# Kernel tuning notes

Measured on AMD Instinct MI355X. Metric: run time of the kernel, lower is better.

## Reference

```python
import jax, jax.numpy as jnp
import numpy as np

NEG_SLOPE = 0.2  # PyG GATConv default leaky_relu slope


def _gat_layer(x, src, dst, n_nodes, W, a_src, a_dst, b, heads, out_ch):
    # x: [N, Fin] -> h: [N, H, C]
    h = (x @ W).reshape(n_nodes, heads, out_ch)
    alpha_s = jnp.einsum('nhc,hc->nh', h, a_src)  # [N, H]
    alpha_d = jnp.einsum('nhc,hc->nh', h, a_dst)  # [N, H]
    e = jax.nn.leaky_relu(alpha_s[src] + alpha_d[dst], NEG_SLOPE)  # [E, H]
    # segment softmax over edges grouped by destination node
    m = jax.ops.segment_max(e, dst, num_segments=n_nodes)          # [N, H]
    e = jnp.exp(e - m[dst])
    denom = jax.ops.segment_sum(e, dst, num_segments=n_nodes)      # [N, H]
    alpha = e / denom[dst]                                          # self-loops guarantee denom > 0
    msg = alpha[:, :, None] * h[src]                                # [E, H, C]
    out = jax.ops.segment_sum(msg, dst, num_segments=n_nodes)      # [N, H, C]
    return out.reshape(n_nodes, heads * out_ch) + b


def reference(x, edge_index, batch, W1, a_src1, a_dst1, b1, W2, a_src2, a_dst2, b2, fc_w, fc_b):
    n_nodes = x.shape[0]
    heads = a_src1.shape[0]
    # PyG GATConv adds self-loops by default
    loops = jnp.arange(n_nodes, dtype=edge_index.dtype)
    src = jnp.concatenate([edge_index[0], loops])
    dst = jnp.concatenate([edge_index[1], loops])

    h = _gat_layer(x, src, dst, n_nodes, W1, a_src1, a_dst1, b1, heads, 64)
    h = jax.nn.relu(h)  # dropout is identity in eval mode
    h = _gat_layer(h, src, dst, n_nodes, W2, a_src2, a_dst2, b2, heads, 16)
    h = jax.nn.relu(h)

    n_graphs = 64
    sums = jax.ops.segment_sum(h, batch, num_segments=n_graphs)                    # [G, 64]
    counts = jax.ops.segment_sum(jnp.ones((n_nodes,), h.dtype), batch, num_segments=n_graphs)
    pooled = sums / jnp.maximum(counts, 1.0)[:, None]                              # global_mean_pool
    return pooled @ fc_w + fc_b


def setup_inputs() -> dict:
    key = jax.random.key(0)
    ks = jax.random.split(key, 12)
    N, E, F_in, G = 50000, 800000, 128, 64
    H = 4
    x = jax.random.normal(ks[0], (N, F_in), jnp.float32)
    edge_index = jax.random.randint(ks[1], (2, E), 0, N, jnp.int32)
    batch = jnp.sort(jax.random.randint(ks[2], (N,), 0, G, jnp.int32))
    s1 = 1.0 / np.sqrt(F_in)
    s2 = 1.0 / np.sqrt(H * 64)
    s3 = 1.0 / np.sqrt(H * 16)
    return {
        'x': x,
        'edge_index': edge_index,
        'batch': batch,
        'W1': jax.random.normal(ks[3], (F_in, H * 64), jnp.float32) * s1,
        'a_src1': jax.random.normal(ks[4], (H, 64), jnp.float32) * s1,
        'a_dst1': jax.random.normal(ks[5], (H, 64), jnp.float32) * s1,
        'b1': jnp.zeros((H * 64,), jnp.float32),
        'W2': jax.random.normal(ks[6], (H * 64, H * 16), jnp.float32) * s2,
        'a_src2': jax.random.normal(ks[7], (H, 16), jnp.float32) * s2,
        'a_dst2': jax.random.normal(ks[8], (H, 16), jnp.float32) * s2,
        'b2': jnp.zeros((H * 16,), jnp.float32),
        'fc_w': jax.random.normal(ks[9], (H * 16, 32), jnp.float32) * s3,
        'fc_b': jnp.zeros((32,), jnp.float32),
    }
```

## Files before the change

### kernel.cpp

```cpp
#include <hip/hip_runtime.h>
#include <hip/hip_bf16.h>
#include <hip/hip_fp16.h>
#include <math.h>

#define HEADS 4
#define CAP 64

typedef _Float16 half8_t __attribute__((ext_vector_type(8)));
typedef float float4_t __attribute__((ext_vector_type(4)));


__global__ void zero_cnt_k(int* cnt, int N) {
    int i = blockIdx.x * blockDim.x + threadIdx.x;
    if (i < N) cnt[i] = 0;
}


__global__ void cvt_w1t_k(const float* __restrict__ W1, _Float16* __restrict__ BT) {
    int k = blockIdx.x;
    int n = threadIdx.x;
    BT[n * 128 + k] = (_Float16)W1[k * 256 + n];
}

__global__ void cvt_w2t_k(const float* __restrict__ W2, _Float16* __restrict__ BT) {
    int n = blockIdx.x;
    int k = threadIdx.x;
    BT[n * 256 + k] = (_Float16)W2[k * 64 + n];
}


__global__ __launch_bounds__(256) void fused_scatter_gemm1_k(
    const int* __restrict__ src, const int* __restrict__ dst,
    int* __restrict__ cnt, unsigned short* __restrict__ slots, int E, int N, int SB,
    const float* __restrict__ A,
    const _Float16* __restrict__ BT,
    __half* __restrict__ hout,
    const float* __restrict__ avs,
    const float* __restrict__ avd,
    float* __restrict__ os,
    float* __restrict__ od, int M) {
    __shared__ _Float16 lds[4 * 16 * 72];

    if ((int)blockIdx.x < SB) {
        int total = E + N;
        int T = SB * 256;
        int t0 = blockIdx.x * 256 + threadIdx.x;
        int d[4], s[4];
        #pragma unroll
        for (int k = 0; k < 4; k++) {
            int i = t0 + k * T;
            if (i < total) {
                if (i < E) { d[k] = dst[i]; s[k] = src[i]; }
                else       { d[k] = i - E;  s[k] = i - E; }
            } else d[k] = -1;
        }
        int p[4];
        #pragma unroll
        for (int k = 0; k < 4; k++) {
            if (d[k] >= 0) p[k] = atomicAdd(&cnt[d[k]], 1);
        }
        #pragma unroll
        for (int k = 0; k < 4; k++) {
            if (d[k] >= 0 && p[k] < CAP)
                slots[(size_t)d[k] * CAP + p[k]] = (unsigned short)s[k];
        }
        return;
    }

    int bx = blockIdx.x - SB;
    int wave = threadIdx.x >> 6;
    int lane = threadIdx.x & 63;
    int q = lane >> 4;
    int c16 = lane & 15;
    int row0 = bx * 64 + wave * 16;

    half8_t a[4];
    int ar = row0 + c16;
    bool avalid = (ar < M);
    const float* ap = A + (size_t)ar * 128;
    #pragma unroll
    for (int ks = 0; ks < 4; ks++) {
        if (avalid) {
            float4 f0 = *(const float4*)(ap + ks * 32 + q * 8);
            float4 f1 = *(const float4*)(ap + ks * 32 + q * 8 + 4);
            half8_t h;
            h[0] = (_Float16)f0.x; h[1] = (_Float16)f0.y;
            h[2] = (_Float16)f0.z; h[3] = (_Float16)f0.w;
            h[4] = (_Float16)f1.x; h[5] = (_Float16)f1.y;
            h[6] = (_Float16)f1.z; h[7] = (_Float16)f1.w;
            a[ks] = h;
        } else {
            a[ks] = (half8_t)(_Float16)0.0f;
        }
    }

    float4_t acc[16];
    #pragma unroll
    for (int ct = 0; ct < 16; ct++) acc[ct] = (float4_t)0.f;

    #pragma unroll
    for (int ks = 0; ks < 4; ks++) {
        #pragma unroll
        for (int ct = 0; ct < 16; ct++) {
            half8_t b = *(const half8_t*)(BT + (size_t)(ct * 16 + c16) * 128 + ks * 32 + q * 8);
            acc[ct] = __builtin_amdgcn_mfma_f32_16x16x32_f16(a[ks], b, acc[ct], 0, 0, 0);
        }
    }

    float psh[4][4] = {}, pdh[4][4] = {};
    #pragma unroll
    for (int ct = 0; ct < 16; ct++) {
        int h = ct >> 2;
        int cih = (ct & 3) * 16 + c16;
        float as_v = avs[h * 64 + cih];
        float ad_v = avd[h * 64 + cih];
        #pragma unroll
        for (int r = 0; r < 4; r++) {
            psh[h][r] = fmaf(acc[ct][r], as_v, psh[h][r]);
            pdh[h][r] = fmaf(acc[ct][r], ad_v, pdh[h][r]);
        }
    }
    #pragma unroll
    for (int h = 0; h < 4; h++) {
        #pragma unroll
        for (int r = 0; r < 4; r++) {
            #pragma unroll
            for (int o = 8; o >= 1; o >>= 1) {
                psh[h][r] += __shfl_down(psh[h][r], o, 16);
                pdh[h][r] += __shfl_down(pdh[h][r], o, 16);
            }
        }
    }
    if (c16 == 0) {
        #pragma unroll
        for (int r = 0; r < 4; r++) {
            int gr = row0 + q * 4 + r;
            if (gr < M) {
                #pragma unroll
                for (int h = 0; h < 4; h++) {
                    os[(size_t)gr * HEADS + h] = psh[h][r];
                    od[(size_t)gr * HEADS + h] = pdh[h][r];
                }
            }
        }
    }

    _Float16* wl = lds + wave * (16 * 72);
    #pragma unroll
    for (int chunk = 0; chunk < 4; chunk++) {
        #pragma unroll
        for (int c4 = 0; c4 < 4; c4++) {
            int ct = chunk * 4 + c4;
            #pragma unroll
            for (int r = 0; r < 4; r++) {
                wl[(q * 4 + r) * 72 + c4 * 16 + c16] = (_Float16)acc[ct][r];
            }
        }
        __syncthreads();
        #pragma unroll
        for (int pass = 0; pass < 2; pass++) {
            int idx8 = pass * 64 + lane;
            int row = idx8 >> 3;
            int col8 = idx8 & 7;
            int gr = row0 + row;
            if (gr < M) {
                *(half8_t*)(hout + (size_t)gr * 256 + chunk * 64 + col8 * 8) =
                    *(const half8_t*)(wl + row * 72 + col8 * 8);
            }
        }
        __syncthreads();
    }
}


__global__ __launch_bounds__(256) void mfma_gemm2_k(
    const _Float16* __restrict__ Ah,
    const _Float16* __restrict__ BT,
    __half* __restrict__ hout,
    const float* __restrict__ avs,
    const float* __restrict__ avd,
    float* __restrict__ os,
    float* __restrict__ od, int M) {
    __shared__ _Float16 lds[4 * 16 * 64];
    int wave = threadIdx.x >> 6;
    int lane = threadIdx.x & 63;
    int q = lane >> 4;
    int c16 = lane & 15;
    int row0 = blockIdx.x * 64 + wave * 16;

    half8_t a[8];
    int ar = row0 + c16;
    bool avalid = (ar < M);
    const _Float16* ap = Ah + (size_t)ar * 256;
    #pragma unroll
    for (int ks = 0; ks < 8; ks++) {
        if (avalid) a[ks] = *(const half8_t*)(ap + ks * 32 + q * 8);
        else        a[ks] = (half8_t)(_Float16)0.0f;
    }

    float4_t acc[4];
    #pragma unroll
    for (int ct = 0; ct < 4; ct++) acc[ct] = (float4_t)0.f;

    #pragma unroll
    for (int ks = 0; ks < 8; ks++) {
        #pragma unroll
        for (int ct = 0; ct < 4; ct++) {
            half8_t b = *(const half8_t*)(BT + (size_t)(ct * 16 + c16) * 256 + ks * 32 + q * 8);
            acc[ct] = __builtin_amdgcn_mfma_f32_16x16x32_f16(a[ks], b, acc[ct], 0, 0, 0);
        }
    }

    float ps[4][4], pd[4][4];
    #pragma unroll
    for (int ct = 0; ct < 4; ct++) {
        float as_v = avs[ct * 16 + c16];
        float ad_v = avd[ct * 16 + c16];
        #pragma unroll
        for (int r = 0; r < 4; r++) {
            ps[ct][r] = acc[ct][r] * as_v;
            pd[ct][r] = acc[ct][r] * ad_v;
            #pragma unroll
            for (int o = 8; o >= 1; o >>= 1) {
                ps[ct][r] += __shfl_down(ps[ct][r], o, 16);
                pd[ct][r] += __shfl_down(pd[ct][r], o, 16);
            }
        }
    }
    if (c16 == 0) {
        #pragma unroll
        for (int r = 0; r < 4; r++) {
            int gr = row0 + q * 4 + r;
            if (gr < M) {
                #pragma unroll
                for (int ct = 0; ct < 4; ct++) {
                    os[(size_t)gr * HEADS + ct] = ps[ct][r];
                    od[(size_t)gr * HEADS + ct] = pd[ct][r];
                }
            }
        }
    }

    _Float16* wl = lds + wave * (16 * 64);
    #pragma unroll
    for (int ct = 0; ct < 4; ct++) {
        #pragma unroll
        for (int r = 0; r < 4; r++) {
            wl[(q * 4 + r) * 64 + ct * 16 + c16] = (_Float16)acc[ct][r];
        }
    }
    __syncthreads();
    #pragma unroll
    for (int pass = 0; pass < 2; pass++) {
        int idx8 = pass * 64 + lane;
        int row = idx8 >> 3;
        int col8 = idx8 & 7;
        int gr = row0 + row;
        if (gr < M) {
            *(half8_t*)(hout + (size_t)gr * 64 + col8 * 8) =
                *(const half8_t*)(wl + row * 64 + col8 * 8);
        }
    }
}


__global__ __launch_bounds__(256) void gat_agg64_f16_k(
    const __half* __restrict__ hsrc,
    const float* __restrict__ as,
    const float* __restrict__ ad,
    const int* __restrict__ cnt,
    const unsigned short* __restrict__ slots,
    const float* __restrict__ bias,
    __half* __restrict__ outh,
    int N) {
    int node = blockIdx.x * 4 + (threadIdx.x >> 6);
    if (node >= N) return;
    int l = threadIdx.x & 63;
    int h = l >> 4;
    int je = l & 15;
    int hb = h << 4;
    int deg = min(cnt[node], CAP);
    const unsigned short* sp = slots + (size_t)node * CAP;
    float adh = ad[(size_t)node * HEADS + h];
    float4 bv = *(const float4*)(bias + l * 4);
    float m = -INFINITY, den = 0.f;
    float4 acc = make_float4(0.f, 0.f, 0.f, 0.f);
    for (int base = 0; base < deg; base += 16) {
        int cl = min(16, deg - base);
        int s = 0;
        float e = -INFINITY;
        if (je < cl) {
            s = sp[base + je];
            float a = as[(size_t)s * HEADS + h] + adh;
            e = (a > 0.f) ? a : 0.2f * a;
        }
        float cmax = e;
        #pragma unroll
        for (int o = 8; o >= 1; o >>= 1) cmax = fmaxf(cmax, __shfl_xor(cmax, o));
        float m_new = fmaxf(m, cmax);
        float p = (je < cl) ? __expf(e - m_new) : 0.f;
        float sum = p;
        #pragma unroll
        for (int o = 8; o >= 1; o >>= 1) sum += __shfl_xor(sum, o);
        float sc = __expf(m - m_new);
        den = den * sc + sum;
        m = m_new;
        acc.x *= sc; acc.y *= sc; acc.z *= sc; acc.w *= sc;
        int j = 0;
        for (; j + 4 <= cl; j += 4) {
            float p0 = __shfl(p, hb + j),     p1 = __shfl(p, hb + j + 1);
            float p2 = __shfl(p, hb + j + 2), p3 = __shfl(p, hb + j + 3);
            int s0 = __shfl(s, hb + j),     s1 = __shfl(s, hb + j + 1);
            int s2 = __shfl(s, hb + j + 2), s3 = __shfl(s, hb + j + 3);
            uint2 r0 = *(const uint2*)(hsrc + (size_t)s0 * 256 + l * 4);
            uint2 r1 = *(const uint2*)(hsrc + (size_t)s1 * 256 + l * 4);
            uint2 r2 = *(const uint2*)(hsrc + (size_t)s2 * 256 + l * 4);
            uint2 r3 = *(const uint2*)(hsrc + (size_t)s3 * 256 + l * 4);
            float2 a0 = __half22float2(*(__half2*)&r0.x), b0 = __half22float2(*(__half2*)&r0.y);
            float2 a1 = __half22float2(*(__half2*)&r1.x), b1 = __half22float2(*(__half2*)&r1.y);
            float2 a2 = __half22float2(*(__half2*)&r2.x), b2 = __half22float2(*(__half2*)&r2.y);
            float2 a3 = __half22float2(*(__half2*)&r3.x), b3 = __half22float2(*(__half2*)&r3.y);
            acc.x = fmaf(p0, a0.x, acc.x); acc.y = fmaf(p0, a0.y, acc.y);
            acc.z = fmaf(p0, b0.x, acc.z); acc.w = fmaf(p0, b0.y, acc.w);
            acc.x = fmaf(p1, a1.x, acc.x); acc.y = fmaf(p1, a1.y, acc.y);
            acc.z = fmaf(p1, b1.x, acc.z); acc.w = fmaf(p1, b1.y, acc.w);
            acc.x = fmaf(p2, a2.x, acc.x); acc.y = fmaf(p2, a2.y, acc.y);
            acc.z = fmaf(p2, b2.x, acc.z); acc.w = fmaf(p2, b2.y, acc.w);
            acc.x = fmaf(p3, a3.x, acc.x); acc.y = fmaf(p3, a3.y, acc.y);
            acc.z = fmaf(p3, b3.x, acc.z); acc.w = fmaf(p3, b3.y, acc.w);
        }
        for (; j < cl; j++) {
            float pj = __shfl(p, hb + j);
            int sj = __shfl(s, hb + j);
            uint2 r0 = *(const uint2*)(hsrc + (size_t)sj * 256 + l * 4);
            float2 a0 = __half22float2(*(__half2*)&r0.x), b0 = __half22float2(*(__half2*)&r0.y);
            acc.x = fmaf(pj, a0.x, acc.x); acc.y = fmaf(pj, a0.y, acc.y);
            acc.z = fmaf(pj, b0.x, acc.z); acc.w = fmaf(pj, b0.y, acc.w);
        }
    }
    float inv = 1.f / den;
    float rx = fmaxf(fmaf(acc.x, inv, bv.x), 0.f);
    float ry = fmaxf(fmaf(acc.y, inv, bv.y), 0.f);
    float rz = fmaxf(fmaf(acc.z, inv, bv.z), 0.f);
    float rw = fmaxf(fmaf(acc.w, inv, bv.w), 0.f);
    __half2* op = (__half2*)(outh + (size_t)node * 256 + l * 4);
    op[0] = __floats2half2_rn(rx, ry);
    op[1] = __floats2half2_rn(rz, rw);
}


__global__ __launch_bounds__(256) void gat_agg16_f16_k(
    const __half* __restrict__ hsrc,
    const float* __restrict__ as,
    const float* __restrict__ ad,
    const int* __restrict__ cnt,
    const unsigned short* __restrict__ slots,
    const float* __restrict__ bias,
    float* __restrict__ out, int N) {
    int node = blockIdx.x * 4 + (threadIdx.x >> 6);
    if (node >= N) return;
    int l = threadIdx.x & 63;
    int ha = l >> 4;
    int je = l & 15;
    int q = l & 15;
    int hh = q >> 2;
    int eg = l >> 4;
    int deg = min(cnt[node], CAP);
    const unsigned short* sp = slots + (size_t)node * CAP;
    float adh = ad[(size_t)node * HEADS + ha];
    float m = -INFINITY, den = 0.f;
    float4 acc = make_float4(0.f, 0.f, 0.f, 0.f);
    for (int base = 0; base < deg; base += 16) {
        int cl = min(16, deg - base);
        int s = 0;
        float e = -INFINITY;
        if (je < cl) {
            s = sp[base + je];
            float a = as[(size_t)s * HEADS + ha] + adh;
            e = (a > 0.f) ? a : 0.2f * a;
        }
        float cmax = e;
        #pragma unroll
        for (int o = 8; o >= 1; o >>= 1) cmax = fmaxf(cmax, __shfl_xor(cmax, o));
        float m_new = fmaxf(m, cmax);
        float p = (je < cl) ? __expf(e - m_new) : 0.f;
        float sum = p;
        #pragma unroll
        for (int o = 8; o >= 1; o >>= 1) sum += __shfl_xor(sum, o);
        float sc = __expf(m - m_new);
        den = den * sc + sum;
        m = m_new;
        float sch = __shfl(sc, hh << 4);
        acc.x *= sch; acc.y *= sch; acc.z *= sch; acc.w *= sch;
        for (int j0 = 0; j0 < cl; j0 += 4) {
            int j = j0 + eg;
            int jc = min(j, cl - 1);
            float pj = __shfl(p, (hh << 4) + jc);
            int sj = __shfl(s, (hh << 4) + jc);
            if (j < cl) {
                uint2 raw = *(const uint2*)(hsrc + (size_t)sj * 64 + q * 4);
                float2 f0 = __half22float2(*(__half2*)&raw.x);
                float2 f1 = __half22float2(*(__half2*)&raw.y);
                acc.x = fmaf(pj, f0.x, acc.x); acc.y = fmaf(pj, f0.y, acc.y);
                acc.z = fmaf(pj, f1.x, acc.z); acc.w = fmaf(pj, f1.y, acc.w);
            }
        }
    }
    acc.x += __shfl_xor(acc.x, 16); acc.y += __shfl_xor(acc.y, 16);
    acc.z += __shfl_xor(acc.z, 16); acc.w += __shfl_xor(acc.w, 16);
    acc.x += __shfl_xor(acc.x, 32); acc.y += __shfl_xor(acc.y, 32);
    acc.z += __shfl_xor(acc.z, 32); acc.w += __shfl_xor(acc.w, 32);
    float denh = __shfl(den, hh << 4);
    if (eg == 0) {
        float inv = 1.f / denh;
        float4 bv = *(const float4*)(bias + q * 4);
        float4 r;
        r.x = fmaxf(fmaf(acc.x, inv, bv.x), 0.f);
        r.y = fmaxf(fmaf(acc.y, inv, bv.y), 0.f);
        r.z = fmaxf(fmaf(acc.z, inv, bv.z), 0.f);
        r.w = fmaxf(fmaf(acc.w, inv, bv.w), 0.f);
        *(float4*)(out + (size_t)node * 64 + q * 4) = r;
    }
}


__global__ void graph_bounds_k(const int* __restrict__ batch, int N, int* __restrict__ bstart) {
    int g = threadIdx.x;
    if (g <= 64) {
        int lo = 0, hi = N;
        while (lo < hi) {
            int mid = (lo + hi) >> 1;
            if (batch[mid] < g) lo = mid + 1; else hi = mid;
        }
        bstart[g] = lo;
    }
}

__global__ void pool_zero_k(float* __restrict__ sums) {
    sums[blockIdx.x * blockDim.x + threadIdx.x] = 0.f;
}

__global__ __launch_bounds__(256) void pool_sum_k(const float* __restrict__ g2,
                                                  const int* __restrict__ batch,
                                                  float* __restrict__ sums, int N) {
    int c = threadIdx.x & 63;
    int r = threadIdx.x >> 6;
    int base = blockIdx.x * 256;
    int lim = min(base + 256, N);
    float acc = 0.f;
    int cur = -1;
    for (int n = base + r; n < lim; n += 4) {
        int g = batch[n];
        if (g != cur) {
            if (cur >= 0) atomicAdd(&sums[cur * 64 + c], acc);
            acc = 0.f;
            cur = g;
        }
        acc += g2[(size_t)n * 64 + c];
    }
    if (cur >= 0) atomicAdd(&sums[cur * 64 + c], acc);
}

__global__ void fc_k(const float* __restrict__ sums, const int* __restrict__ bstart,
                     const float* __restrict__ w, const float* __restrict__ b,
                     float* __restrict__ out) {
    int g = blockIdx.x, o = threadIdx.x;
    float cnt_ = (float)max(bstart[g + 1] - bstart[g], 1);
    float inv = 1.f / cnt_;
    float acc = b[o];
    for (int k = 0; k < 64; k++) acc = fmaf(sums[g * 64 + k] * inv, w[k * 32 + o], acc);
    out[g * 32 + o] = acc;
}


static inline size_t align_up(size_t x, size_t a) { return (x + a - 1) & ~(a - 1); }

extern "C" void kernel_launch(void* const* d_in, const int* in_sizes, int n_in,
                              void* d_out, int out_size, void* d_ws, size_t ws_size,
                              hipStream_t stream) {
    const float* x      = (const float*)d_in[0];
    const int*   ei     = (const int*)d_in[1];
    const int*   batch  = (const int*)d_in[2];
    const float* W1     = (const float*)d_in[3];
    const float* a_src1 = (const float*)d_in[4];
    const float* a_dst1 = (const float*)d_in[5];
    const float* b1     = (const float*)d_in[6];
    const float* W2     = (const float*)d_in[7];
    const float* a_src2 = (const float*)d_in[8];
    const float* a_dst2 = (const float*)d_in[9];
    const float* b2     = (const float*)d_in[10];
    const float* fc_w   = (const float*)d_in[11];
    const float* fc_b   = (const float*)d_in[12];
    float* out = (float*)d_out;

    const int N = in_sizes[2];
    const int E = in_sizes[1] / 2;
    const int F_in = in_sizes[0] / N;
    const int D1 = HEADS * 64;
    const int D2 = HEADS * 16;

    const int* src = ei;
    const int* dst = ei + E;

    char* w = (char*)d_ws;
    size_t off = 0;
    auto alloc = [&](size_t bytes) {
        size_t p = off;
        off = align_up(off + bytes, 256);
        return (void*)(w + p);
    };
    int* cnt    = (int*)alloc((size_t)N * 4);
    unsigned short* slots = (unsigned short*)alloc((size_t)N * CAP * 2);
    int* bstart = (int*)alloc(65 * 4);
    float* pooled = (float*)alloc(64 * 64 * 4);
    float* as1  = (float*)alloc((size_t)N * HEADS * 4);
    float* ad1  = (float*)alloc((size_t)N * HEADS * 4);
    float* as2  = (float*)alloc((size_t)N * HEADS * 4);
    float* ad2  = (float*)alloc((size_t)N * HEADS * 4);
    __half* h1h = (__half*)alloc((size_t)N * D1 * 2);
    __half* g1h = (__half*)alloc((size_t)N * D1 * 2);
    __half* h2h = (__half*)alloc((size_t)N * D2 * 2);
    float* g2   = (float*)alloc((size_t)N * D2 * 4);
    _Float16* w1t = (_Float16*)alloc((size_t)F_in * D1 * 2);
    _Float16* w2t = (_Float16*)alloc((size_t)D1 * D2 * 2);

    zero_cnt_k<<<(N + 255) / 256, 256, 0, stream>>>(cnt, N);
    cvt_w1t_k<<<F_in, D1, 0, stream>>>(W1, w1t);
    cvt_w2t_k<<<D2, D1, 0, stream>>>(W2, w2t);

    const int SB = (E + N + 1023) / 1024;
    const int GB = (N + 63) / 64;
    fused_scatter_gemm1_k<<<SB + GB, 256, 0, stream>>>(
        src, dst, cnt, slots, E, N, SB,
        x, w1t, h1h, a_src1, a_dst1, as1, ad1, N);

    gat_agg64_f16_k<<<(N + 3) / 4, 256, 0, stream>>>(h1h, as1, ad1, cnt, slots, b1, g1h, N);

    mfma_gemm2_k<<<(N + 63) / 64, 256, 0, stream>>>((const _Float16*)g1h, w2t, h2h,
                                                    a_src2, a_dst2, as2, ad2, N);
    gat_agg16_f16_k<<<(N + 3) / 4, 256, 0, stream>>>(h2h, as2, ad2, cnt, slots, b2, g2, N);

    graph_bounds_k<<<1, 128, 0, stream>>>(batch, N, bstart);
    pool_zero_k<<<16, 256, 0, stream>>>(pooled);
    pool_sum_k<<<(N + 255) / 256, 256, 0, stream>>>(g2, batch, pooled, N);
    fc_k<<<64, 32, 0, stream>>>(pooled, bstart, fc_w, fc_b, out);
}
```

Baseline: 336.4 us.

## Partition edge scatter by destination range and pre-insert self-loops in init

```diff
diff --git a/kernel.cpp b/kernel.cpp
--- a/kernel.cpp
+++ b/kernel.cpp
@@ -10,9 +10,12 @@
 typedef float float4_t __attribute__((ext_vector_type(4)));
 
 
-__global__ void zero_cnt_k(int* cnt, int N) {
+__global__ void init_cnt_k(int* cnt, unsigned short* slots, int N) {
     int i = blockIdx.x * blockDim.x + threadIdx.x;
-    if (i < N) cnt[i] = 0;
+    if (i < N) {
+        cnt[i] = 1;
+        slots[(size_t)i * CAP] = (unsigned short)i;
+    }
 }
 
 
@@ -42,27 +45,19 @@
     __shared__ _Float16 lds[4 * 16 * 72];
 
     if ((int)blockIdx.x < SB) {
-        int total = E + N;
-        int T = SB * 256;
-        int t0 = blockIdx.x * 256 + threadIdx.x;
-        int d[4], s[4];
-        #pragma unroll
-        for (int k = 0; k < 4; k++) {
-            int i = t0 + k * T;
-            if (i < total) {
-                if (i < E) { d[k] = dst[i]; s[k] = src[i]; }
-                else       { d[k] = i - E;  s[k] = i - E; }
-            } else d[k] = -1;
-        }
-        int p[4];
-        #pragma unroll
-        for (int k = 0; k < 4; k++) {
-            if (d[k] >= 0) p[k] = atomicAdd(&cnt[d[k]], 1);
-        }
-        #pragma unroll
-        for (int k = 0; k < 4; k++) {
-            if (d[k] >= 0 && p[k] < CAP)
-                slots[(size_t)d[k] * CAP + p[k]] = (unsigned short)s[k];
+        int p = blockIdx.x & 7;
+        int bp = blockIdx.x >> 3;
+        int SBP = SB >> 3;
+        int T = SBP * 256;
+        int pstart = (int)(((long long)p * N) >> 3);
+        int pend   = (int)(((long long)(p + 1) * N) >> 3);
+        for (int i = bp * 256 + (int)threadIdx.x; i < E; i += T) {
+            int d = dst[i];
+            int s = src[i];
+            if (d >= pstart && d < pend) {
+                int pos = atomicAdd(&cnt[d], 1);
+                if (pos < CAP) slots[(size_t)d * CAP + pos] = (unsigned short)s;
+            }
         }
         return;
     }
@@ -524,11 +519,11 @@
     _Float16* w1t = (_Float16*)alloc((size_t)F_in * D1 * 2);
     _Float16* w2t = (_Float16*)alloc((size_t)D1 * D2 * 2);
 
-    zero_cnt_k<<<(N + 255) / 256, 256, 0, stream>>>(cnt, N);
+    init_cnt_k<<<(N + 255) / 256, 256, 0, stream>>>(cnt, slots, N);
     cvt_w1t_k<<<F_in, D1, 0, stream>>>(W1, w1t);
     cvt_w2t_k<<<D2, D1, 0, stream>>>(W2, w2t);
 
-    const int SB = (E + N + 1023) / 1024;
+    const int SB = 832;
     const int GB = (N + 63) / 64;
     fused_scatter_gemm1_k<<<SB + GB, 256, 0, stream>>>(
         src, dst, cnt, slots, E, N, SB,
```

Result: no change. 333.3 us (-0.9%).

## Split layer-1 aggregation per head across XCDs and pre-insert self-loops

Applied to the files above, without the earlier changes.

```diff
diff --git a/kernel.cpp b/kernel.cpp
--- a/kernel.cpp
+++ b/kernel.cpp
@@ -10,9 +10,12 @@
 typedef float float4_t __attribute__((ext_vector_type(4)));
 
 
-__global__ void zero_cnt_k(int* cnt, int N) {
+__global__ void init_cnt_k(int* cnt, unsigned short* slots, int N) {
     int i = blockIdx.x * blockDim.x + threadIdx.x;
-    if (i < N) cnt[i] = 0;
+    if (i < N) {
+        cnt[i] = 1;
+        slots[(size_t)i * CAP] = (unsigned short)i;
+    }
 }
 
 
@@ -31,7 +34,7 @@
 
 __global__ __launch_bounds__(256) void fused_scatter_gemm1_k(
     const int* __restrict__ src, const int* __restrict__ dst,
-    int* __restrict__ cnt, unsigned short* __restrict__ slots, int E, int N, int SB,
+    int* __restrict__ cnt, unsigned short* __restrict__ slots, int E, int SB,
     const float* __restrict__ A,
     const _Float16* __restrict__ BT,
     __half* __restrict__ hout,
@@ -42,25 +45,22 @@
     __shared__ _Float16 lds[4 * 16 * 72];
 
     if ((int)blockIdx.x < SB) {
-        int total = E + N;
         int T = SB * 256;
         int t0 = blockIdx.x * 256 + threadIdx.x;
-        int d[4], s[4];
-        #pragma unroll
-        for (int k = 0; k < 4; k++) {
+        int d[8], s[8];
+        #pragma unroll
+        for (int k = 0; k < 8; k++) {
             int i = t0 + k * T;
-            if (i < total) {
-                if (i < E) { d[k] = dst[i]; s[k] = src[i]; }
-                else       { d[k] = i - E;  s[k] = i - E; }
-            } else d[k] = -1;
-        }
-        int p[4];
-        #pragma unroll
-        for (int k = 0; k < 4; k++) {
+            if (i < E) { d[k] = dst[i]; s[k] = src[i]; }
+            else d[k] = -1;
+        }
+        int p[8];
+        #pragma unroll
+        for (int k = 0; k < 8; k++) {
             if (d[k] >= 0) p[k] = atomicAdd(&cnt[d[k]], 1);
         }
         #pragma unroll
-        for (int k = 0; k < 4; k++) {
+        for (int k = 0; k < 8; k++) {
             if (d[k] >= 0 && p[k] < CAP)
                 slots[(size_t)d[k] * CAP + p[k]] = (unsigned short)s[k];
         }
@@ -264,7 +264,7 @@
 }
 
 
-__global__ __launch_bounds__(256) void gat_agg64_f16_k(
+__global__ __launch_bounds__(256) void gat_agg64_xcd_k(
     const __half* __restrict__ hsrc,
     const float* __restrict__ as,
     const float* __restrict__ ad,
@@ -273,32 +273,34 @@
     const float* __restrict__ bias,
     __half* __restrict__ outh,
     int N) {
-    int node = blockIdx.x * 4 + (threadIdx.x >> 6);
+    int t7 = blockIdx.x & 7;
+    int head = t7 >> 1;
+    int g = ((int)(blockIdx.x >> 3)) * 2 + (t7 & 1);
+    int node = g * 4 + (threadIdx.x >> 6);
     if (node >= N) return;
     int l = threadIdx.x & 63;
-    int h = l >> 4;
-    int je = l & 15;
-    int hb = h << 4;
+    int q = l & 15;
+    int eg = l >> 4;
     int deg = min(cnt[node], CAP);
     const unsigned short* sp = slots + (size_t)node * CAP;
-    float adh = ad[(size_t)node * HEADS + h];
-    float4 bv = *(const float4*)(bias + l * 4);
+    float adh = ad[(size_t)node * HEADS + head];
     float m = -INFINITY, den = 0.f;
     float4 acc = make_float4(0.f, 0.f, 0.f, 0.f);
+    const __half* hbase = hsrc + head * 64 + (size_t)q * 4;
     for (int base = 0; base < deg; base += 16) {
         int cl = min(16, deg - base);
         int s = 0;
         float e = -INFINITY;
-        if (je < cl) {
-            s = sp[base + je];
-            float a = as[(size_t)s * HEADS + h] + adh;
+        if (q < cl) {
+            s = sp[base + q];
+            float a = as[(size_t)s * HEADS + head] + adh;
             e = (a > 0.f) ? a : 0.2f * a;
         }
         float cmax = e;
         #pragma unroll
         for (int o = 8; o >= 1; o >>= 1) cmax = fmaxf(cmax, __shfl_xor(cmax, o));
         float m_new = fmaxf(m, cmax);
-        float p = (je < cl) ? __expf(e - m_new) : 0.f;
+        float p = (q < cl) ? __expf(e - m_new) : 0.f;
         float sum = p;
         #pragma unroll
         for (int o = 8; o >= 1; o >>= 1) sum += __shfl_xor(sum, o);
@@ -306,46 +308,35 @@
         den = den * sc + sum;
         m = m_new;
         acc.x *= sc; acc.y *= sc; acc.z *= sc; acc.w *= sc;
-        int j = 0;
-        for (; j + 4 <= cl; j += 4) {
-            float p0 = __shfl(p, hb + j),     p1 = __shfl(p, hb + j + 1);
-            float p2 = __shfl(p, hb + j + 2), p3 = __shfl(p, hb + j + 3);
-            int s0 = __shfl(s, hb + j),     s1 = __shfl(s, hb + j + 1);
-            int s2 = __shfl(s, hb + j + 2), s3 = __shfl(s, hb + j + 3);
-            uint2 r0 = *(const uint2*)(hsrc + (size_t)s0 * 256 + l * 4);
-            uint2 r1 = *(const uint2*)(hsrc + (size_t)s1 * 256 + l * 4);
-            uint2 r2 = *(const uint2*)(hsrc + (size_t)s2 * 256 + l * 4);
-            uint2 r3 = *(const uint2*)(hsrc + (size_t)s3 * 256 + l * 4);
-            float2 a0 = __half22float2(*(__half2*)&r0.x), b0 = __half22float2(*(__half2*)&r0.y);
-            float2 a1 = __half22float2(*(__half2*)&r1.x), b1 = __half22float2(*(__half2*)&r1.y);
-            float2 a2 = __half22float2(*(__half2*)&r2.x), b2 = __half22float2(*(__half2*)&r2.y);
-            float2 a3 = __half22float2(*(__half2*)&r3.x), b3 = __half22float2(*(__half2*)&r3.y);
-            acc.x = fmaf(p0, a0.x, acc.x); acc.y = fmaf(p0, a0.y, acc.y);
-            acc.z = fmaf(p0, b0.x, acc.z); acc.w = fmaf(p0, b0.y, acc.w);
-            acc.x = fmaf(p1, a1.x, acc.x); acc.y = fmaf(p1, a1.y, acc.y);
-            acc.z = fmaf(p1, b1.x, acc.z); acc.w = fmaf(p1, b1.y, acc.w);
-            acc.x = fmaf(p2, a2.x, acc.x); acc.y = fmaf(p2, a2.y, acc.y);
-            acc.z = fmaf(p2, b2.x, acc.z); acc.w = fmaf(p2, b2.y, acc.w);
-            acc.x = fmaf(p3, a3.x, acc.x); acc.y = fmaf(p3, a3.y, acc.y);
-            acc.z = fmaf(p3, b3.x, acc.z); acc.w = fmaf(p3, b3.y, acc.w);
-        }
-        for (; j < cl; j++) {
-            float pj = __shfl(p, hb + j);
-            int sj = __shfl(s, hb + j);
-            uint2 r0 = *(const uint2*)(hsrc + (size_t)sj * 256 + l * 4);
-            float2 a0 = __half22float2(*(__half2*)&r0.x), b0 = __half22float2(*(__half2*)&r0.y);
-            acc.x = fmaf(pj, a0.x, acc.x); acc.y = fmaf(pj, a0.y, acc.y);
-            acc.z = fmaf(pj, b0.x, acc.z); acc.w = fmaf(pj, b0.y, acc.w);
-        }
-    }
-    float inv = 1.f / den;
-    float rx = fmaxf(fmaf(acc.x, inv, bv.x), 0.f);
-    float ry = fmaxf(fmaf(acc.y, inv, bv.y), 0.f);
-    float rz = fmaxf(fmaf(acc.z, inv, bv.z), 0.f);
-    float rw = fmaxf(fmaf(acc.w, inv, bv.w), 0.f);
-    __half2* op = (__half2*)(outh + (size_t)node * 256 + l * 4);
-    op[0] = __floats2half2_rn(rx, ry);
-    op[1] = __floats2half2_rn(rz, rw);
+        for (int j0 = 0; j0 < cl; j0 += 4) {
+            int j = j0 + eg;
+            int jc = min(j, cl - 1);
+            float pj = __shfl(p, jc);
+            int sj = __shfl(s, jc);
+            if (j < cl) {
+                uint2 raw = *(const uint2*)(hbase + (size_t)sj * 256);
+                float2 f0 = __half22float2(*(__half2*)&raw.x);
+                float2 f1 = __half22float2(*(__half2*)&raw.y);
+                acc.x = fmaf(pj, f0.x, acc.x); acc.y = fmaf(pj, f0.y, acc.y);
+                acc.z = fmaf(pj, f1.x, acc.z); acc.w = fmaf(pj, f1.y, acc.w);
+            }
+        }
+    }
+    acc.x += __shfl_xor(acc.x, 16); acc.y += __shfl_xor(acc.y, 16);
+    acc.z += __shfl_xor(acc.z, 16); acc.w += __shfl_xor(acc.w, 16);
+    acc.x += __shfl_xor(acc.x, 32); acc.y += __shfl_xor(acc.y, 32);
+    acc.z += __shfl_xor(acc.z, 32); acc.w += __shfl_xor(acc.w, 32);
+    if (eg == 0) {
+        float inv = 1.f / den;
+        float4 bv = *(const float4*)(bias + head * 64 + q * 4);
+        float rx = fmaxf(fmaf(acc.x, inv, bv.x), 0.f);
+        float ry = fmaxf(fmaf(acc.y, inv, bv.y), 0.f);
+        float rz = fmaxf(fmaf(acc.z, inv, bv.z), 0.f);
+        float rw = fmaxf(fmaf(acc.w, inv, bv.w), 0.f);
+        __half2* op = (__half2*)(outh + (size_t)node * 256 + head * 64 + q * 4);
+        op[0] = __floats2half2_rn(rx, ry);
+        op[1] = __floats2half2_rn(rz, rw);
+    }
 }
 
 
@@ -524,17 +515,21 @@
     _Float16* w1t = (_Float16*)alloc((size_t)F_in * D1 * 2);
     _Float16* w2t = (_Float16*)alloc((size_t)D1 * D2 * 2);
 
-    zero_cnt_k<<<(N + 255) / 256, 256, 0, stream>>>(cnt, N);
+    init_cnt_k<<<(N + 255) / 256, 256, 0, stream>>>(cnt, slots, N);
     cvt_w1t_k<<<F_in, D1, 0, stream>>>(W1, w1t);
     cvt_w2t_k<<<D2, D1, 0, stream>>>(W2, w2t);
 
-    const int SB = (E + N + 1023) / 1024;
+    const int SB = (E + 2047) / 2048;
     const int GB = (N + 63) / 64;
     fused_scatter_gemm1_k<<<SB + GB, 256, 0, stream>>>(
-        src, dst, cnt, slots, E, N, SB,
+        src, dst, cnt, slots, E, SB,
         x, w1t, h1h, a_src1, a_dst1, as1, ad1, N);
 
-    gat_agg64_f16_k<<<(N + 3) / 4, 256, 0, stream>>>(h1h, as1, ad1, cnt, slots, b1, g1h, N);
+    {
+        int ngroups = (N + 3) / 4;
+        int bps = (ngroups + 1) / 2;
+        gat_agg64_xcd_k<<<8 * bps, 256, 0, stream>>>(h1h, as1, ad1, cnt, slots, b1, g1h, N);
+    }
 
     mfma_gemm2_k<<<(N + 63) / 64, 256, 0, stream>>>((const _Float16*)g1h, w2t, h2h,
                                                     a_src2, a_dst2, as2, ad2, N);
```

Result: slower. 387.8 us (+15.3%).
